# Kernel optimization log

Hardware: AMD Instinct MI355X
Metric: run time of the kernel (lower is better)

## Reference

```python
import jax, jax.numpy as jnp
import numpy as np

BSZ, SEQ, DIM = 4, 4096, 1024
MEASURE_DIM = 64
TOPK = 16
NUM_TARGETS = 1


def fwht(x):
    """Fast Walsh-Hadamard transform over last dim (power of two), orthonormal scaling."""
    n = x.shape[-1]
    y = x
    h = 1
    while h < n:
        y = y.reshape(*y.shape[:-1], -1, 2, h)
        a, b = y[..., 0, :], y[..., 1, :]
        y = jnp.concatenate((a + b, a - b), axis=-1)
        y = y.reshape(*x.shape[:-1], n)
        h *= 2
    return y * (n ** -0.5)


def setup_inputs() -> dict:
    key = jax.random.key(0)
    kx, kg, ka, kt, ks, kp = jax.random.split(key, 6)
    x = jax.random.normal(kx, (BSZ, SEQ, DIM), dtype=jnp.float32)
    gates = jax.random.uniform(kg, (BSZ, NUM_TARGETS, MEASURE_DIM), dtype=jnp.float32) + 0.5
    alpha = jax.random.uniform(ka, (BSZ, NUM_TARGETS, 1), dtype=jnp.float32) * 0.1
    tau = jax.random.uniform(kt, (BSZ, NUM_TARGETS, 1), dtype=jnp.float32) * 0.02
    signs = jnp.where(jax.random.uniform(ks, (DIM,)) > 0.5, 1.0, -1.0).astype(jnp.float32)
    perm = jax.random.permutation(kp, DIM).astype(jnp.int32)
    inv_perm = jnp.argsort(perm).astype(jnp.int32)
    return {"x": x, "gates": gates, "alpha": alpha, "tau": tau,
            "signs": signs, "perm": perm, "inv_perm": inv_perm, "target_idx": 0}


def reference(x, gates, alpha, tau, signs, perm, inv_perm, target_idx):
    signs_ = signs.astype(x.dtype)
    # ---- sense: sign flip -> permute -> FWHT -> truncate ----
    y = jnp.take((x * signs_[None, None, :]), perm, axis=-1)
    z = fwht(y)[..., :MEASURE_DIM]  # [B, S, m]
    # ---- shrink (topk mode) ----
    gate = gates[:, target_idx][:, None, :]            # [B, 1, m]
    alpha_t = alpha[:, target_idx][:, None, :]         # [B, 1, 1]
    tau_t = jnp.abs(tau[:, target_idx])[:, None, :]    # [B, 1, 1]
    gated = gate * z
    agated = jnp.abs(gated)
    _, idx = jax.lax.top_k(agated, TOPK)               # [B, S, k]
    mask = jax.nn.one_hot(idx, MEASURE_DIM, dtype=gated.dtype).sum(-2)  # [B, S, m]
    sparse = jnp.where((mask > 0) & (agated >= tau_t), gated, jnp.zeros_like(gated))
    zs = alpha_t * sparse
    # ---- reconstruct: pad -> FWHT -> inverse permute -> sign flip ----
    full = jnp.zeros((*zs.shape[:-1], DIM), dtype=zs.dtype).at[..., :MEASURE_DIM].set(zs)
    r = jnp.take(fwht(full), inv_perm, axis=-1) * signs_[None, None, :]
    return x + r
```

## Files before the change

kernel.cpp:

```cpp
#include <hip/hip_runtime.h>

#define SEQ 4096
#define DIM 1024
#define MD 64
#define TOPK 16
#define WPB 2
#define RPW 4
#define RPB (WPB * RPW)

typedef float nfloat4 __attribute__((ext_vector_type(4)));

__device__ __forceinline__ int swzU(int u) { return u ^ ((u >> 3) & 7); }

__global__ __launch_bounds__(WPB * 64) void csa_kernel(
    const float* __restrict__ x,
    const float* __restrict__ gates,
    const float* __restrict__ alpha,
    const float* __restrict__ tau,
    const float* __restrict__ signs,
    const int*   __restrict__ perm,
    const int*   __restrict__ inv_perm,
    const int*   __restrict__ target_idx,
    float*       __restrict__ out)
{
    __shared__ float lds[RPB * DIM];

    const int lane = threadIdx.x & 63;
    const int wv   = threadIdx.x >> 6;
    const int r0   = (blockIdx.x * WPB + wv) * RPW;
    const int b    = r0 >> 12;

    float4* Lw = (float4*)(lds + wv * (RPW * DIM));

    #pragma unroll
    for (int c = 0; c < 4; ++c) {
        const float4 sg = ((const float4*)signs)[c * 64 + lane];
        float4 a[RPW];
        #pragma unroll
        for (int r = 0; r < RPW; ++r) {
            const float4 xv = ((const float4*)(x + (size_t)(r0 + r) * DIM))[c * 64 + lane];
            a[r].x = xv.x * sg.x; a[r].y = xv.y * sg.y;
            a[r].z = xv.z * sg.z; a[r].w = xv.w * sg.w;
        }
        const int d0 = c * 256 + 4 * lane;
        float4 u0, u1, u2, u3;
        u0.x = a[0].x; u0.y = a[1].x; u0.z = a[2].x; u0.w = a[3].x;
        u1.x = a[0].y; u1.y = a[1].y; u1.z = a[2].y; u1.w = a[3].y;
        u2.x = a[0].z; u2.y = a[1].z; u2.z = a[2].z; u2.w = a[3].z;
        u3.x = a[0].w; u3.y = a[1].w; u3.z = a[2].w; u3.w = a[3].w;
        Lw[swzU(d0 + 0)] = u0;
        Lw[swzU(d0 + 1)] = u1;
        Lw[swzU(d0 + 2)] = u2;
        Lw[swzU(d0 + 3)] = u3;
    }

    float s0 = 0.f, s1 = 0.f, s2 = 0.f, s3 = 0.f;
    #pragma unroll
    for (int k = 0; k < 16; ++k) {
        const int p = perm[lane + 64 * k];
        const float4 q = Lw[swzU(p)];
        s0 += q.x; s1 += q.y; s2 += q.z; s3 += q.w;
    }

    float v0 = s0, v1 = s1, v2 = s2, v3 = s3;
    #pragma unroll
    for (int bit = 1; bit < MD; bit <<= 1) {
        const float o0 = __shfl_xor(v0, bit, 64);
        const float o1 = __shfl_xor(v1, bit, 64);
        const float o2 = __shfl_xor(v2, bit, 64);
        const float o3 = __shfl_xor(v3, bit, 64);
        v0 = (lane & bit) ? (o0 - v0) : (v0 + o0);
        v1 = (lane & bit) ? (o1 - v1) : (v1 + o1);
        v2 = (lane & bit) ? (o2 - v2) : (v2 + o2);
        v3 = (lane & bit) ? (o3 - v3) : (v3 + o3);
    }

    const int   ti   = target_idx[0];
    const float gate = gates[(b + ti) * MD + lane];
    const float tauv = fabsf(tau[b + ti]);
    const float al   = alpha[b + ti];

    const float g0 = gate * v0 * 0.03125f;
    const float g1 = gate * v1 * 0.03125f;
    const float g2 = gate * v2 * 0.03125f;
    const float g3 = gate * v3 * 0.03125f;
    const float ag0 = fabsf(g0), ag1 = fabsf(g1), ag2 = fabsf(g2), ag3 = fabsf(g3);

    const unsigned ka0 = __float_as_uint(ag0);
    const unsigned ka1 = __float_as_uint(ag1);
    const unsigned ka2 = __float_as_uint(ag2);
    const unsigned ka3 = __float_as_uint(ag3);
    unsigned T0 = 0u, T1 = 0u, T2 = 0u, T3 = 0u;
    #pragma unroll
    for (int bit = 30; bit >= 0; --bit) {
        const unsigned c0 = T0 | (1u << bit);
        const unsigned c1 = T1 | (1u << bit);
        const unsigned c2 = T2 | (1u << bit);
        const unsigned c3 = T3 | (1u << bit);
        if (__popcll(__ballot(ka0 >= c0)) >= TOPK) T0 = c0;
        if (__popcll(__ballot(ka1 >= c1)) >= TOPK) T1 = c1;
        if (__popcll(__ballot(ka2 >= c2)) >= TOPK) T2 = c2;
        if (__popcll(__ballot(ka3 >= c3)) >= TOPK) T3 = c3;
    }
    const unsigned long long lm = (1ull << lane) - 1ull;
    const int ngt0 = __popcll(__ballot(ka0 > T0));
    const int ngt1 = __popcll(__ballot(ka1 > T1));
    const int ngt2 = __popcll(__ballot(ka2 > T2));
    const int ngt3 = __popcll(__ballot(ka3 > T3));
    const int er0 = __popcll(__ballot(ka0 == T0) & lm);
    const int er1 = __popcll(__ballot(ka1 == T1) & lm);
    const int er2 = __popcll(__ballot(ka2 == T2) & lm);
    const int er3 = __popcll(__ballot(ka3 == T3) & lm);
    const bool k0 = (ka0 > T0) || ((ka0 == T0) && (er0 < TOPK - ngt0));
    const bool k1 = (ka1 > T1) || ((ka1 == T1) && (er1 < TOPK - ngt1));
    const bool k2 = (ka2 > T2) || ((ka2 == T2) && (er2 < TOPK - ngt2));
    const bool k3 = (ka3 > T3) || ((ka3 == T3) && (er3 < TOPK - ngt3));

    float zs0 = (k0 && ag0 >= tauv) ? al * g0 : 0.f;
    float zs1 = (k1 && ag1 >= tauv) ? al * g1 : 0.f;
    float zs2 = (k2 && ag2 >= tauv) ? al * g2 : 0.f;
    float zs3 = (k3 && ag3 >= tauv) ? al * g3 : 0.f;

    #pragma unroll
    for (int bit = 1; bit < MD; bit <<= 1) {
        const float o0 = __shfl_xor(zs0, bit, 64);
        const float o1 = __shfl_xor(zs1, bit, 64);
        const float o2 = __shfl_xor(zs2, bit, 64);
        const float o3 = __shfl_xor(zs3, bit, 64);
        zs0 = (lane & bit) ? (o0 - zs0) : (zs0 + o0);
        zs1 = (lane & bit) ? (o1 - zs1) : (zs1 + o1);
        zs2 = (lane & bit) ? (o2 - zs2) : (zs2 + o2);
        zs3 = (lane & bit) ? (o3 - zs3) : (zs3 + o3);
    }
    const float w0 = zs0 * 0.03125f;
    const float w1 = zs1 * 0.03125f;
    const float w2 = zs2 * 0.03125f;
    const float w3 = zs3 * 0.03125f;

    #pragma unroll
    for (int c = 0; c < 4; ++c) {
        const int4   ip = ((const int4*)inv_perm)[c * 64 + lane];
        const float4 sg = ((const float4*)signs)[c * 64 + lane];
        const int d0 = c * 256 + 4 * lane;
        const float4 t0 = Lw[swzU(d0 + 0)];
        const float4 t1 = Lw[swzU(d0 + 1)];
        const float4 t2 = Lw[swzU(d0 + 2)];
        const float4 t3 = Lw[swzU(d0 + 3)];
        const int b0 = ip.x & 63, b1 = ip.y & 63, b2 = ip.z & 63, b3 = ip.w & 63;

        nfloat4 o0, o1, o2, o3;
        o0.x = sg.x * (t0.x + __shfl(w0, b0, 64));
        o0.y = sg.y * (t1.x + __shfl(w0, b1, 64));
        o0.z = sg.z * (t2.x + __shfl(w0, b2, 64));
        o0.w = sg.w * (t3.x + __shfl(w0, b3, 64));
        o1.x = sg.x * (t0.y + __shfl(w1, b0, 64));
        o1.y = sg.y * (t1.y + __shfl(w1, b1, 64));
        o1.z = sg.z * (t2.y + __shfl(w1, b2, 64));
        o1.w = sg.w * (t3.y + __shfl(w1, b3, 64));
        o2.x = sg.x * (t0.z + __shfl(w2, b0, 64));
        o2.y = sg.y * (t1.z + __shfl(w2, b1, 64));
        o2.z = sg.z * (t2.z + __shfl(w2, b2, 64));
        o2.w = sg.w * (t3.z + __shfl(w2, b3, 64));
        o3.x = sg.x * (t0.w + __shfl(w3, b0, 64));
        o3.y = sg.y * (t1.w + __shfl(w3, b1, 64));
        o3.z = sg.z * (t2.w + __shfl(w3, b2, 64));
        o3.w = sg.w * (t3.w + __shfl(w3, b3, 64));

        __builtin_nontemporal_store(o0, &((nfloat4*)(out + (size_t)(r0 + 0) * DIM))[c * 64 + lane]);
        __builtin_nontemporal_store(o1, &((nfloat4*)(out + (size_t)(r0 + 1) * DIM))[c * 64 + lane]);
        __builtin_nontemporal_store(o2, &((nfloat4*)(out + (size_t)(r0 + 2) * DIM))[c * 64 + lane]);
        __builtin_nontemporal_store(o3, &((nfloat4*)(out + (size_t)(r0 + 3) * DIM))[c * 64 + lane]);
    }
}

extern "C" void kernel_launch(void* const* d_in, const int* in_sizes, int n_in,
                              void* d_out, int out_size, void* d_ws, size_t ws_size,
                              hipStream_t stream) {
    const float* x        = (const float*)d_in[0];
    const float* gates    = (const float*)d_in[1];
    const float* alpha    = (const float*)d_in[2];
    const float* tau      = (const float*)d_in[3];
    const float* signs    = (const float*)d_in[4];
    const int*   perm     = (const int*)d_in[5];
    const int*   inv_perm = (const int*)d_in[6];
    const int*   tgt      = (const int*)d_in[7];
    float*       out      = (float*)d_out;

    const int rows = 4 * SEQ;
    csa_kernel<<<rows / RPB, WPB * 64, 0, stream>>>(x, gates, alpha, tau, signs,
                                                    perm, inv_perm, tgt, out);
}
```

Measured before the change: 126.8 us.

## Halve LDS footprint by processing rows in pairs and rereading x from global

Replaces the 4-row interleaved swizzled LDS buffer with two plain per-row buffers per wave, processed in two passes of two rows each, with perm indices held in registers. The final output now rereads x from global memory instead of keeping it in LDS, so LDS per block drops from 32KB to 16KB and occupancy can rise. The cost is a second read of x, which may hit in cache, plus scalar LDS gathers in place of float4 gathers.

```diff
diff --git a/kernel.cpp b/kernel.cpp
--- a/kernel.cpp
+++ b/kernel.cpp
@@ -9,8 +9,6 @@
 #define RPB (WPB * RPW)
 
 typedef float nfloat4 __attribute__((ext_vector_type(4)));
-
-__device__ __forceinline__ int swzU(int u) { return u ^ ((u >> 3) & 7); }
 
 __global__ __launch_bounds__(WPB * 64) void csa_kernel(
     const float* __restrict__ x,
@@ -23,43 +21,63 @@
     const int*   __restrict__ target_idx,
     float*       __restrict__ out)
 {
-    __shared__ float lds[RPB * DIM];
+    __shared__ float y[WPB * 2][DIM];
 
     const int lane = threadIdx.x & 63;
     const int wv   = threadIdx.x >> 6;
     const int r0   = (blockIdx.x * WPB + wv) * RPW;
     const int b    = r0 >> 12;
 
-    float4* Lw = (float4*)(lds + wv * (RPW * DIM));
+    float* y0 = y[wv * 2 + 0];
+    float* y1 = y[wv * 2 + 1];
+
+    int pk[16];
+    #pragma unroll
+    for (int k = 0; k < 16; ++k) pk[k] = perm[lane + 64 * k];
 
     #pragma unroll
     for (int c = 0; c < 4; ++c) {
         const float4 sg = ((const float4*)signs)[c * 64 + lane];
-        float4 a[RPW];
-        #pragma unroll
-        for (int r = 0; r < RPW; ++r) {
-            const float4 xv = ((const float4*)(x + (size_t)(r0 + r) * DIM))[c * 64 + lane];
-            a[r].x = xv.x * sg.x; a[r].y = xv.y * sg.y;
-            a[r].z = xv.z * sg.z; a[r].w = xv.w * sg.w;
-        }
-        const int d0 = c * 256 + 4 * lane;
-        float4 u0, u1, u2, u3;
-        u0.x = a[0].x; u0.y = a[1].x; u0.z = a[2].x; u0.w = a[3].x;
-        u1.x = a[0].y; u1.y = a[1].y; u1.z = a[2].y; u1.w = a[3].y;
-        u2.x = a[0].z; u2.y = a[1].z; u2.z = a[2].z; u2.w = a[3].z;
-        u3.x = a[0].w; u3.y = a[1].w; u3.z = a[2].w; u3.w = a[3].w;
-        Lw[swzU(d0 + 0)] = u0;
-        Lw[swzU(d0 + 1)] = u1;
-        Lw[swzU(d0 + 2)] = u2;
-        Lw[swzU(d0 + 3)] = u3;
-    }
-
-    float s0 = 0.f, s1 = 0.f, s2 = 0.f, s3 = 0.f;
+        const float4 xa = ((const float4*)(x + (size_t)(r0 + 0) * DIM))[c * 64 + lane];
+        const float4 xb = ((const float4*)(x + (size_t)(r0 + 1) * DIM))[c * 64 + lane];
+        float4 a, bq;
+        a.x  = xa.x * sg.x; a.y  = xa.y * sg.y; a.z  = xa.z * sg.z; a.w  = xa.w * sg.w;
+        bq.x = xb.x * sg.x; bq.y = xb.y * sg.y; bq.z = xb.z * sg.z; bq.w = xb.w * sg.w;
+        ((float4*)y0)[c * 64 + lane] = a;
+        ((float4*)y1)[c * 64 + lane] = bq;
+    }
+
+    float4 xc[4], xd[4];
+    #pragma unroll
+    for (int c = 0; c < 4; ++c) {
+        xc[c] = ((const float4*)(x + (size_t)(r0 + 2) * DIM))[c * 64 + lane];
+        xd[c] = ((const float4*)(x + (size_t)(r0 + 3) * DIM))[c * 64 + lane];
+    }
+
+    float s0 = 0.f, s1 = 0.f;
     #pragma unroll
     for (int k = 0; k < 16; ++k) {
-        const int p = perm[lane + 64 * k];
-        const float4 q = Lw[swzU(p)];
-        s0 += q.x; s1 += q.y; s2 += q.z; s3 += q.w;
+        s0 += y0[pk[k]];
+        s1 += y1[pk[k]];
+    }
+
+    #pragma unroll
+    for (int c = 0; c < 4; ++c) {
+        const float4 sg = ((const float4*)signs)[c * 64 + lane];
+        float4 a, bq;
+        a.x  = xc[c].x * sg.x; a.y  = xc[c].y * sg.y;
+        a.z  = xc[c].z * sg.z; a.w  = xc[c].w * sg.w;
+        bq.x = xd[c].x * sg.x; bq.y = xd[c].y * sg.y;
+        bq.z = xd[c].z * sg.z; bq.w = xd[c].w * sg.w;
+        ((float4*)y0)[c * 64 + lane] = a;
+        ((float4*)y1)[c * 64 + lane] = bq;
+    }
+
+    float s2 = 0.f, s3 = 0.f;
+    #pragma unroll
+    for (int k = 0; k < 16; ++k) {
+        s2 += y0[pk[k]];
+        s3 += y1[pk[k]];
     }
 
     float v0 = s0, v1 = s1, v2 = s2, v3 = s3;
@@ -141,30 +159,29 @@
     for (int c = 0; c < 4; ++c) {
         const int4   ip = ((const int4*)inv_perm)[c * 64 + lane];
         const float4 sg = ((const float4*)signs)[c * 64 + lane];
-        const int d0 = c * 256 + 4 * lane;
-        const float4 t0 = Lw[swzU(d0 + 0)];
-        const float4 t1 = Lw[swzU(d0 + 1)];
-        const float4 t2 = Lw[swzU(d0 + 2)];
-        const float4 t3 = Lw[swzU(d0 + 3)];
+        const float4 xr0 = ((const float4*)(x + (size_t)(r0 + 0) * DIM))[c * 64 + lane];
+        const float4 xr1 = ((const float4*)(x + (size_t)(r0 + 1) * DIM))[c * 64 + lane];
+        const float4 xr2 = ((const float4*)(x + (size_t)(r0 + 2) * DIM))[c * 64 + lane];
+        const float4 xr3 = ((const float4*)(x + (size_t)(r0 + 3) * DIM))[c * 64 + lane];
         const int b0 = ip.x & 63, b1 = ip.y & 63, b2 = ip.z & 63, b3 = ip.w & 63;
 
         nfloat4 o0, o1, o2, o3;
-        o0.x = sg.x * (t0.x + __shfl(w0, b0, 64));
-        o0.y = sg.y * (t1.x + __shfl(w0, b1, 64));
-        o0.z = sg.z * (t2.x + __shfl(w0, b2, 64));
-        o0.w = sg.w * (t3.x + __shfl(w0, b3, 64));
-        o1.x = sg.x * (t0.y + __shfl(w1, b0, 64));
-        o1.y = sg.y * (t1.y + __shfl(w1, b1, 64));
-        o1.z = sg.z * (t2.y + __shfl(w1, b2, 64));
-        o1.w = sg.w * (t3.y + __shfl(w1, b3, 64));
-        o2.x = sg.x * (t0.z + __shfl(w2, b0, 64));
-        o2.y = sg.y * (t1.z + __shfl(w2, b1, 64));
-        o2.z = sg.z * (t2.z + __shfl(w2, b2, 64));
-        o2.w = sg.w * (t3.z + __shfl(w2, b3, 64));
-        o3.x = sg.x * (t0.w + __shfl(w3, b0, 64));
-        o3.y = sg.y * (t1.w + __shfl(w3, b1, 64));
-        o3.z = sg.z * (t2.w + __shfl(w3, b2, 64));
-        o3.w = sg.w * (t3.w + __shfl(w3, b3, 64));
+        o0.x = xr0.x + sg.x * __shfl(w0, b0, 64);
+        o0.y = xr0.y + sg.y * __shfl(w0, b1, 64);
+        o0.z = xr0.z + sg.z * __shfl(w0, b2, 64);
+        o0.w = xr0.w + sg.w * __shfl(w0, b3, 64);
+        o1.x = xr1.x + sg.x * __shfl(w1, b0, 64);
+        o1.y = xr1.y + sg.y * __shfl(w1, b1, 64);
+        o1.z = xr1.z + sg.z * __shfl(w1, b2, 64);
+        o1.w = xr1.w + sg.w * __shfl(w1, b3, 64);
+        o2.x = xr2.x + sg.x * __shfl(w2, b0, 64);
+        o2.y = xr2.y + sg.y * __shfl(w2, b1, 64);
+        o2.z = xr2.z + sg.z * __shfl(w2, b2, 64);
+        o2.w = xr2.w + sg.w * __shfl(w2, b3, 64);
+        o3.x = xr3.x + sg.x * __shfl(w3, b0, 64);
+        o3.y = xr3.y + sg.y * __shfl(w3, b1, 64);
+        o3.z = xr3.z + sg.z * __shfl(w3, b2, 64);
+        o3.w = xr3.w + sg.w * __shfl(w3, b3, 64);
 
         __builtin_nontemporal_store(o0, &((nfloat4*)(out + (size_t)(r0 + 0) * DIM))[c * 64 + lane]);
         __builtin_nontemporal_store(o1, &((nfloat4*)(out + (size_t)(r0 + 1) * DIM))[c * 64 + lane]);
```

New measurement: 133.0 us. 1.05x slower.
